# Kernel tuning notes

Measured on AMD Instinct MI355X. Metric: run time of the kernel, lower is better.

The kernel has to match this reference:

```python
import jax, jax.numpy as jnp
import numpy as np

L, D, H, FF = 6, 1024, 16, 4096
HD = D // H
EPS = 1e-5


def _ln(x, g, b):
    m = jnp.mean(x, axis=-1, keepdims=True)
    v = jnp.var(x, axis=-1, keepdims=True)
    return (x - m) * jax.lax.rsqrt(v + EPS) * g + b


def _heads(t, S, B):  # [S,B,D] -> [B*H,S,HD]
    return t.reshape(S, B * H, HD).swapaxes(0, 1)


def _attn(q, k, v, mask):
    # q,k,v: [B*H, Sq/Sk, HD]; q pre-scaled
    scores = jnp.einsum('bqd,bkd->bqk', q, k)
    if mask is not None:
        scores = scores + mask  # broadcast [1,Sq,Sk]
    p = jax.nn.softmax(scores, axis=-1)
    return jnp.einsum('bqk,bkd->bqd', p, v)


def _self_attn(x, w_qkv, b_qkv, w_out, b_out, mask):
    S, B, _ = x.shape
    qkv = x @ w_qkv.T + b_qkv  # [S,B,3D]
    q, k, v = jnp.split(qkv, 3, axis=-1)
    q = q * (HD ** -0.5)
    a = _attn(_heads(q, S, B), _heads(k, S, B), _heads(v, S, B), mask)
    a = a.swapaxes(0, 1).reshape(S, B, D)
    return a @ w_out.T + b_out


def _cross_attn(x, mem, w_q, b_q, w_kv, b_kv, w_out, b_out):
    S, B, _ = x.shape
    Sm = mem.shape[0]
    q = (x @ w_q.T + b_q) * (HD ** -0.5)
    kv = mem @ w_kv.T + b_kv  # [Sm,B,2D]
    k, v = jnp.split(kv, 2, axis=-1)
    a = _attn(_heads(q, S, B), _heads(k, Sm, B), _heads(v, Sm, B), None)
    a = a.swapaxes(0, 1).reshape(S, B, D)
    return a @ w_out.T + b_out


def _ffn(x, w1, b1, w2, b2):
    h = jax.nn.gelu(x @ w1.T + b1, approximate=False)
    return h @ w2.T + b2


def setup_inputs() -> dict:
    key = jax.random.key(0)
    ks = iter(jax.random.split(key, 64))
    def p(*shape, s=0.02):
        return (jax.random.normal(next(ks), shape, dtype=jnp.float32) * s)
    inp = {
        'src': jax.random.normal(next(ks), (512, 8, D), dtype=jnp.float32),
        'tgt': jax.random.normal(next(ks), (512, 8, D), dtype=jnp.float32),
        # encoder params (stacked over L layers)
        'enc_qkv_w': p(L, 3 * D, D), 'enc_qkv_b': p(L, 3 * D),
        'enc_out_w': p(L, D, D), 'enc_out_b': p(L, D),
        'enc_ln1_g': jnp.ones((L, D)), 'enc_ln1_b': jnp.zeros((L, D)),
        'enc_fc1_w': p(L, FF, D), 'enc_fc1_b': p(L, FF),
        'enc_fc2_w': p(L, D, FF), 'enc_fc2_b': p(L, D),
        'enc_ln2_g': jnp.ones((L, D)), 'enc_ln2_b': jnp.zeros((L, D)),
        'enc_norm_g': jnp.ones((D,)), 'enc_norm_b': jnp.zeros((D,)),
        # decoder params
        'dec_qkv_w': p(L, 3 * D, D), 'dec_qkv_b': p(L, 3 * D),
        'dec_sout_w': p(L, D, D), 'dec_sout_b': p(L, D),
        'dec_ln1_g': jnp.ones((L, D)), 'dec_ln1_b': jnp.zeros((L, D)),
        'dec_q_w': p(L, D, D), 'dec_q_b': p(L, D),
        'dec_kv_w': p(L, 2 * D, D), 'dec_kv_b': p(L, 2 * D),
        'dec_cout_w': p(L, D, D), 'dec_cout_b': p(L, D),
        'dec_ln2_g': jnp.ones((L, D)), 'dec_ln2_b': jnp.zeros((L, D)),
        'dec_fc1_w': p(L, FF, D), 'dec_fc1_b': p(L, FF),
        'dec_fc2_w': p(L, D, FF), 'dec_fc2_b': p(L, D),
        'dec_ln3_g': jnp.ones((L, D)), 'dec_ln3_b': jnp.zeros((L, D)),
        'dec_norm_g': jnp.ones((D,)), 'dec_norm_b': jnp.zeros((D,)),
    }
    return inp


def reference(src, tgt,
              enc_qkv_w, enc_qkv_b, enc_out_w, enc_out_b,
              enc_ln1_g, enc_ln1_b, enc_fc1_w, enc_fc1_b,
              enc_fc2_w, enc_fc2_b, enc_ln2_g, enc_ln2_b,
              enc_norm_g, enc_norm_b,
              dec_qkv_w, dec_qkv_b, dec_sout_w, dec_sout_b,
              dec_ln1_g, dec_ln1_b, dec_q_w, dec_q_b,
              dec_kv_w, dec_kv_b, dec_cout_w, dec_cout_b,
              dec_ln2_g, dec_ln2_b, dec_fc1_w, dec_fc1_b,
              dec_fc2_w, dec_fc2_b, dec_ln3_g, dec_ln3_b,
              dec_norm_g, dec_norm_b):
    St = tgt.shape[0]
    # causal additive mask [1,St,St]
    causal = jnp.where(jnp.tril(jnp.ones((St, St), dtype=bool)), 0.0, -jnp.inf)
    causal = causal[None].astype(src.dtype)

    # ---- encoder ----
    x = src
    for i in range(L):
        x = x + _self_attn(_ln(x, enc_ln1_g[i], enc_ln1_b[i]),
                           enc_qkv_w[i], enc_qkv_b[i], enc_out_w[i], enc_out_b[i], None)
        x = x + _ffn(_ln(x, enc_ln2_g[i], enc_ln2_b[i]),
                     enc_fc1_w[i], enc_fc1_b[i], enc_fc2_w[i], enc_fc2_b[i])
    memory = _ln(x, enc_norm_g, enc_norm_b)

    # ---- decoder ----
    y = tgt
    for i in range(L):
        y = y + _self_attn(_ln(y, dec_ln1_g[i], dec_ln1_b[i]),
                           dec_qkv_w[i], dec_qkv_b[i], dec_sout_w[i], dec_sout_b[i], causal)
        y = y + _cross_attn(_ln(y, dec_ln2_g[i], dec_ln2_b[i]), memory,
                            dec_q_w[i], dec_q_b[i], dec_kv_w[i], dec_kv_b[i],
                            dec_cout_w[i], dec_cout_b[i])
        y = y + _ffn(_ln(y, dec_ln3_g[i], dec_ln3_b[i]),
                     dec_fc1_w[i], dec_fc1_b[i], dec_fc2_w[i], dec_fc2_b[i])
    return _ln(y, dec_norm_g, dec_norm_b)
```

## Files before the change

kernel.cpp:

```cpp
#include <hip/hip_runtime.h>

typedef __attribute__((ext_vector_type(4))) float f32x4;
typedef __attribute__((ext_vector_type(8))) short short8;
typedef unsigned int u32;
typedef unsigned short u16;
typedef __attribute__((ext_vector_type(2))) u32 u32x2;
typedef __attribute__((ext_vector_type(4))) u32 u32x4;

#define DEV __device__ __forceinline__
#define SB0  __builtin_amdgcn_sched_barrier(0)
#define HBAR asm volatile("s_barrier" ::: "memory")

DEV u16 f2b(float f){
  u32 u = __builtin_bit_cast(u32, f);
  u32 r = u + 0x7fffu + ((u >> 16) & 1u);
  return (u16)(r >> 16);
}
DEV u32 pk2(float a, float b){ return (u32)f2b(a) | ((u32)f2b(b) << 16); }

DEV void gload16(const void* g, void* l){
  __builtin_amdgcn_global_load_lds((const __attribute__((address_space(1))) void*)g,
                                   (__attribute__((address_space(3))) void*)l, 16, 0, 0);
}
DEV u32 lds_addr(void* p){
  return (u32)(unsigned long long)(__attribute__((address_space(3))) char*)p;
}

__global__ __launch_bounds__(256) void cvt_k(const float* __restrict__ in,
                                             u16* __restrict__ out, int n8)
{
  int i = blockIdx.x*256 + threadIdx.x;
  const int stride = gridDim.x*256;
  for (; i < n8; i += stride){
    const float4 a = ((const float4*)in)[2*i];
    const float4 b = ((const float4*)in)[2*i+1];
    u32x4 r;
    r.x = pk2(a.x,a.y); r.y = pk2(a.z,a.w);
    r.z = pk2(b.x,b.y); r.w = pk2(b.z,b.w);
    ((u32x4*)out)[i] = r;
  }
}

template<int OUT_F32>
__global__ __launch_bounds__(256) void ln_k(const float* __restrict__ x,
    const float* __restrict__ gam, const float* __restrict__ bet,
    void* __restrict__ out)
{
  const int row = blockIdx.x, tid = threadIdx.x;
  const float4 v = ((const float4*)(x + row*1024))[tid];
  float s = (v.x + v.y) + (v.z + v.w);
  float q = (v.x*v.x + v.y*v.y) + (v.z*v.z + v.w*v.w);
  #pragma unroll
  for (int m = 1; m < 64; m <<= 1){ s += __shfl_xor(s, m); q += __shfl_xor(q, m); }
  __shared__ float ps[4], pq[4];
  if ((tid & 63) == 0){ ps[tid>>6] = s; pq[tid>>6] = q; }
  __syncthreads();
  s = (ps[0]+ps[1]) + (ps[2]+ps[3]);
  q = (pq[0]+pq[1]) + (pq[2]+pq[3]);
  const float mean = s * (1.f/1024.f);
  const float var  = q * (1.f/1024.f) - mean*mean;
  const float rstd = rsqrtf(var + 1e-5f);
  const float4 gg = ((const float4*)gam)[tid];
  const float4 bb = ((const float4*)bet)[tid];
  const float o0 = (v.x-mean)*rstd*gg.x + bb.x;
  const float o1 = (v.y-mean)*rstd*gg.y + bb.y;
  const float o2 = (v.z-mean)*rstd*gg.z + bb.z;
  const float o3 = (v.w-mean)*rstd*gg.w + bb.w;
  if (OUT_F32){
    float4 r; r.x=o0; r.y=o1; r.z=o2; r.w=o3;
    ((float4*)out)[row*256 + tid] = r;
  } else {
    u32x2 r; r.x = pk2(o0,o1); r.y = pk2(o2,o3);
    ((u32x2*)out)[row*256 + tid] = r;
  }
}

template<int DO_GELU>
__global__ __launch_bounds__(512,2) void gemm256_k(
    const u16* __restrict__ A, const u16* __restrict__ W,
    const float* __restrict__ bias, u16* __restrict__ Cout,
    int M, int N, int K)
{
  __shared__ char lds[131072];
  const int tid = threadIdx.x;
  const int lane = tid & 63, wid = tid >> 6;
  const int wr = wid >> 2, wc = wid & 3;
  const int g = lane >> 4, c16 = lane & 15;

  const u32 nwg = gridDim.x * gridDim.y;
  u32 flat = blockIdx.x + gridDim.x * blockIdx.y;
  {
    const u32 q = nwg >> 3, r = nwg & 7;
    const u32 xcd = flat & 7, idx = flat >> 3;
    flat = (xcd < r ? xcd*(q+1) : r*(q+1) + (xcd-r)*q) + idx;
  }
  const int m0 = (int)(flat % gridDim.x) * 256;
  const int n0 = (int)(flat / gridDim.x) * 256;

  f32x4 acc[8][4];
  #pragma unroll
  for (int m = 0; m < 8; m++)
    #pragma unroll
    for (int n = 0; n < 4; n++) acc[m][n] = (f32x4){0.f,0.f,0.f,0.f};

  const int srow = tid >> 3, schk = tid & 7;
  const int scg = schk ^ (srow & 7);
  const u16* aS = A + (size_t)(m0 + srow)*K + scg*8;
  const u16* wS = W + (size_t)(n0 + srow)*K + scg*8;

  auto SG = [&](const u16* base, int regionOff, int sb, int half, int i, int kk){
    gload16(base + (size_t)(half*128 + i*64)*K + kk,
            lds + sb*65536 + regionOff + half*16384 + i*8192 + tid*16);
  };
  short8 af[4][2], bf[4][2];
  auto LDA4 = [&](char* bufA, int mbase){
    #pragma unroll
    for (int i = 0; i < 4; i++){
      const int r = (mbase + i)*16 + c16;
      const int rx = r & 7;
      af[i][0] = *(const short8*)(bufA + r*128 + ((g ^ rx) << 4));
      af[i][1] = *(const short8*)(bufA + r*128 + (((4 + g) ^ rx) << 4));
    }
  };
  auto LDB2 = [&](char* bufB, int nbase){
    #pragma unroll
    for (int i = 0; i < 2; i++){
      const int r = (wc & 1)*64 + (nbase + i)*16 + c16;
      const int rx = r & 7;
      bf[nbase+i][0] = *(const short8*)(bufB + r*128 + ((g ^ rx) << 4));
      bf[nbase+i][1] = *(const short8*)(bufB + r*128 + (((4 + g) ^ rx) << 4));
    }
  };

  const int NT = K >> 6;
  SG(wS, 32768, 0, 0, 0, 0); SG(wS, 32768, 0, 0, 1, 0);
  SG(wS, 32768, 0, 1, 0, 0); SG(wS, 32768, 0, 1, 1, 0);
  SG(aS, 0,     0, 0, 0, 0); SG(aS, 0,     0, 0, 1, 0);
  SG(aS, 0,     0, 1, 0, 0); SG(aS, 0,     0, 1, 1, 0);
  asm volatile("s_waitcnt vmcnt(1)" ::: "memory");
  HBAR;

  for (int t = 0; t < NT; ++t){
    const int b = t & 1, sb = b ^ 1;
    const int skk = (t+1) << 6;
    const bool st = (t+1 < NT);
    char* bufA = lds + b*65536 + wr*16384;
    char* bufB = lds + b*65536 + 32768 + (wc >> 1)*16384;

    LDA4(bufA, 0); LDB2(bufB, 0);
    if (st){ SG(wS, 32768, sb, 0, 0, skk); SG(wS, 32768, sb, 0, 1, skk); }
    HBAR;
    asm volatile("s_waitcnt lgkmcnt(0)" ::: "memory"); SB0;
    __builtin_amdgcn_s_setprio(1);
    #pragma unroll
    for (int ks = 0; ks < 2; ks++)
      #pragma unroll
      for (int i = 0; i < 4; i++)
        #pragma unroll
        for (int j = 0; j < 2; j++)
          acc[i][j] = __builtin_amdgcn_mfma_f32_16x16x32_bf16(af[i][ks], bf[j][ks], acc[i][j], 0,0,0);
    __builtin_amdgcn_s_setprio(0);
    LDB2(bufB, 2);
    if (st){ SG(wS, 32768, sb, 1, 0, skk); SG(wS, 32768, sb, 1, 1, skk); }
    HBAR;
    asm volatile("s_waitcnt lgkmcnt(0)" ::: "memory"); SB0;
    __builtin_amdgcn_s_setprio(1);
    #pragma unroll
    for (int ks = 0; ks < 2; ks++)
      #pragma unroll
      for (int i = 0; i < 4; i++)
        #pragma unroll
        for (int j = 2; j < 4; j++)
          acc[i][j] = __builtin_amdgcn_mfma_f32_16x16x32_bf16(af[i][ks], bf[j][ks], acc[i][j], 0,0,0);
    __builtin_amdgcn_s_setprio(0);
    if (st) asm volatile("s_waitcnt vmcnt(4)" ::: "memory");
    else    asm volatile("s_waitcnt vmcnt(0)" ::: "memory");
    HBAR;
    LDA4(bufA, 4);
    if (st){ SG(aS, 0, sb, 0, 0, skk); SG(aS, 0, sb, 0, 1, skk); }
    asm volatile("s_waitcnt lgkmcnt(0)" ::: "memory"); SB0;
    __builtin_amdgcn_s_setprio(1);
    #pragma unroll
    for (int ks = 0; ks < 2; ks++)
      #pragma unroll
      for (int i = 0; i < 4; i++)
        #pragma unroll
        for (int j = 0; j < 2; j++)
          acc[4+i][j] = __builtin_amdgcn_mfma_f32_16x16x32_bf16(af[i][ks], bf[j][ks], acc[4+i][j], 0,0,0);
    __builtin_amdgcn_s_setprio(0);
    if (st){ SG(aS, 0, sb, 1, 0, skk); SG(aS, 0, sb, 1, 1, skk); }
    HBAR;
    __builtin_amdgcn_s_setprio(1);
    #pragma unroll
    for (int ks = 0; ks < 2; ks++)
      #pragma unroll
      for (int i = 0; i < 4; i++)
        #pragma unroll
        for (int j = 2; j < 4; j++)
          acc[4+i][j] = __builtin_amdgcn_mfma_f32_16x16x32_bf16(af[i][ks], bf[j][ks], acc[4+i][j], 0,0,0);
    __builtin_amdgcn_s_setprio(0);
    if (st) asm volatile("s_waitcnt vmcnt(1)" ::: "memory");
    HBAR;
  }

  #pragma unroll
  for (int n = 0; n < 4; n++){
    const int col = n0 + wc*64 + n*16 + c16;
    const float bv = bias[col];
    #pragma unroll
    for (int m = 0; m < 8; m++){
      const int rbase = m0 + wr*128 + m*16 + g*4;
      #pragma unroll
      for (int r = 0; r < 4; r++){
        float v = acc[m][n][r] + bv;
        if (DO_GELU) v = 0.5f*v*(1.f + erff(v*0.70710678118654752f));
        Cout[(size_t)(rbase + r)*N + col] = f2b(v);
      }
    }
  }
}

template<int DO_GELU, int DO_RES, int OUT_F32>
__global__ __launch_bounds__(512,2) void gemm128p_k(
    const u16* __restrict__ A, const u16* __restrict__ W,
    const float* __restrict__ bias, const float* __restrict__ res,
    void* __restrict__ Cout, int M, int N, int K)
{
  __shared__ char lds[65536];
  const int tid = threadIdx.x;
  const int lane = tid & 63, wid = tid >> 6;
  const int wr = wid >> 2, wc = wid & 3;
  const int g = lane >> 4, c16 = lane & 15;

  const u32 nwg = gridDim.x * gridDim.y;
  u32 flat = blockIdx.x + gridDim.x * blockIdx.y;
  {
    const u32 q = nwg >> 3, r = nwg & 7;
    const u32 xcd = flat & 7, idx = flat >> 3;
    flat = (xcd < r ? xcd*(q+1) : r*(q+1) + (xcd-r)*q) + idx;
  }
  const int n0 = (int)(flat % gridDim.x) * 128;
  const int m0 = (int)(flat / gridDim.x) * 128;

  f32x4 acc[4][2];
  #pragma unroll
  for (int m = 0; m < 4; m++)
    #pragma unroll
    for (int n = 0; n < 2; n++) acc[m][n] = (f32x4){0.f,0.f,0.f,0.f};

  const int srow = tid >> 3, schk = tid & 7;
  const int scg = schk ^ (srow & 7);
  const u16* aS = A + (size_t)(m0 + srow)*K + scg*8;
  const u16* wS = W + (size_t)(n0 + srow)*K + scg*8;

  auto SG = [&](const u16* base, int regionOff, int sb, int i, int kk){
    gload16(base + (size_t)(i*64)*K + kk,
            lds + sb*32768 + regionOff + i*8192 + tid*16);
  };
  short8 af[2][2], af2[2][2], bf[2][2];
  auto LDA = [&](short8 (*dst)[2], char* bufA, int mbase){
    #pragma unroll
    for (int i = 0; i < 2; i++){
      const int r = wr*64 + (mbase + i)*16 + c16;
      const int rx = r & 7;
      dst[i][0] = *(const short8*)(bufA + r*128 + ((g ^ rx) << 4));
      dst[i][1] = *(const short8*)(bufA + r*128 + (((4 + g) ^ rx) << 4));
    }
  };
  auto LDB = [&](char* bufB){
    #pragma unroll
    for (int i = 0; i < 2; i++){
      const int r = wc*32 + i*16 + c16;
      const int rx = r & 7;
      bf[i][0] = *(const short8*)(bufB + r*128 + ((g ^ rx) << 4));
      bf[i][1] = *(const short8*)(bufB + r*128 + (((4 + g) ^ rx) << 4));
    }
  };

  const int NT = K >> 6;
  SG(wS, 16384, 0, 0, 0); SG(wS, 16384, 0, 1, 0);
  SG(aS, 0,     0, 0, 0); SG(aS, 0,     0, 1, 0);

  for (int t = 0; t < NT; ++t){
    const int b = t & 1, sb = b ^ 1;
    const int skk = (t+1) << 6;
    const bool st = (t+1 < NT);
    char* bufA = lds + b*32768;
    char* bufB = lds + b*32768 + 16384;

    if (st){ SG(wS, 16384, sb, 0, skk); SG(wS, 16384, sb, 1, skk); }
    if (st) asm volatile("s_waitcnt vmcnt(2)" ::: "memory");
    else    asm volatile("s_waitcnt vmcnt(0)" ::: "memory");
    HBAR;
    LDA(af, bufA, 0); LDB(bufB);
    if (st){ SG(aS, 0, sb, 0, skk); SG(aS, 0, sb, 1, skk); }
    asm volatile("s_waitcnt lgkmcnt(0)" ::: "memory"); SB0;
    __builtin_amdgcn_s_setprio(1);
    #pragma unroll
    for (int ks = 0; ks < 2; ks++)
      #pragma unroll
      for (int i = 0; i < 2; i++)
        #pragma unroll
        for (int j = 0; j < 2; j++)
          acc[i][j] = __builtin_amdgcn_mfma_f32_16x16x32_bf16(af[i][ks], bf[j][ks], acc[i][j], 0,0,0);
    __builtin_amdgcn_s_setprio(0);
    LDA(af2, bufA, 2);
    asm volatile("s_waitcnt lgkmcnt(0)" ::: "memory"); SB0;
    __builtin_amdgcn_s_setprio(1);
    #pragma unroll
    for (int ks = 0; ks < 2; ks++)
      #pragma unroll
      for (int i = 0; i < 2; i++)
        #pragma unroll
        for (int j = 0; j < 2; j++)
          acc[2+i][j] = __builtin_amdgcn_mfma_f32_16x16x32_bf16(af2[i][ks], bf[j][ks], acc[2+i][j], 0,0,0);
    __builtin_amdgcn_s_setprio(0);
    HBAR;
  }

  #pragma unroll
  for (int n = 0; n < 2; n++){
    const int col = n0 + wc*32 + n*16 + c16;
    const float bv = bias[col];
    #pragma unroll
    for (int m = 0; m < 4; m++){
      const int rbase = m0 + wr*64 + m*16 + g*4;
      #pragma unroll
      for (int r = 0; r < 4; r++){
        float v = acc[m][n][r] + bv;
        if (DO_GELU) v = 0.5f*v*(1.f + erff(v*0.70710678118654752f));
        if (DO_RES)  v += res[(size_t)(rbase + r)*N + col];
        if (OUT_F32) ((float*)Cout)[(size_t)(rbase + r)*N + col] = v;
        else         ((u16*)Cout)[(size_t)(rbase + r)*N + col] = f2b(v);
      }
    }
  }
}

template<int CAUSAL>
__global__ __launch_bounds__(256,4) void attn_k(
    const u16* __restrict__ Qb, int qB, int qS,
    const u16* __restrict__ Kb, int kB, int kS,
    const u16* __restrict__ Vb, int vB, int vS,
    u16* __restrict__ Ob, int oB, int oS, float scale)
{
  __shared__ char smem[32768];
  const int tid = threadIdx.x;
  const int lane = tid & 63, w = tid >> 6;
  const int g = lane >> 4, c16 = lane & 15;
  const int qt = blockIdx.x, bh = blockIdx.y;
  const int b = bh >> 4, h = bh & 15;
  const u16* Q  = Qb + b*qB + h*64;
  const u16* Kp = Kb + b*kB + h*64;
  const u16* Vp = Vb + b*vB + h*64;
  u16*       Op = Ob + b*oB + h*64;

  const int qrow = qt*64 + w*16 + c16;
  const short8 bq0 = *(const short8*)(Q + qrow*qS + g*8);
  const short8 bq1 = *(const short8*)(Q + qrow*qS + 32 + g*8);

  f32x4 o[4];
  #pragma unroll
  for (int d = 0; d < 4; d++) o[d] = (f32x4){0.f,0.f,0.f,0.f};
  float mrun = -__builtin_inff(), lrun = 0.f;

  const int srow = tid >> 3, schk = tid & 7;
  const u16* kSrc = Kp + srow*kS + (schk ^ (srow & 7))*8;
  const u16* vSrc = Vp + srow*vS + schk*8;
  const u32 vtr0 = lds_addr(smem) + 16384 + (8*g + (c16 >> 2))*128 + (c16 & 3)*8;

  auto STAGE = [&](int p, int j0){
    char* kb = smem + p*8192 + w*1024;
    char* vb = smem + 16384 + p*8192 + w*1024;
    gload16(kSrc + (size_t)j0*kS, kb);
    gload16(kSrc + (size_t)(j0+32)*kS, kb + 4096);
    gload16(vSrc + (size_t)j0*vS, vb);
    gload16(vSrc + (size_t)(j0+32)*vS, vb + 4096);
  };
  auto COMPUTE = [&](int p, int j0){
    char* Ks = smem + p*8192;
    f32x4 st[4];
    #pragma unroll
    for (int t = 0; t < 4; t++){
      const int row = t*16 + c16;
      const int rx = row & 7;
      const short8 ka0 = *(const short8*)(Ks + row*128 + ((g ^ rx) << 4));
      const short8 ka1 = *(const short8*)(Ks + row*128 + (((4 + g) ^ rx) << 4));
      f32x4 z = (f32x4){0.f,0.f,0.f,0.f};
      z = __builtin_amdgcn_mfma_f32_16x16x32_bf16(ka0, bq0, z, 0,0,0);
      z = __builtin_amdgcn_mfma_f32_16x16x32_bf16(ka1, bq1, z, 0,0,0);
      st[t] = z;
    }
    float mloc = -__builtin_inff();
    #pragma unroll
    for (int t = 0; t < 4; t++)
      #pragma unroll
      for (int r = 0; r < 4; r++){
        float sv = st[t][r]*scale;
        if (CAUSAL){ if (j0 + t*16 + g*4 + r > qrow) sv = -__builtin_inff(); }
        st[t][r] = sv;
        mloc = fmaxf(mloc, sv);
      }
    mloc = fmaxf(mloc, __shfl_xor(mloc, 16));
    mloc = fmaxf(mloc, __shfl_xor(mloc, 32));
    const float mnew = fmaxf(mrun, mloc);
    const float corr = __expf(mrun - mnew);
    float psum = 0.f;
    u32 pk[4][2];
    #pragma unroll
    for (int t = 0; t < 4; t++){
      const float p0 = __expf(st[t][0]-mnew), p1 = __expf(st[t][1]-mnew);
      const float p2 = __expf(st[t][2]-mnew), p3 = __expf(st[t][3]-mnew);
      psum += (p0+p1) + (p2+p3);
      pk[t][0] = pk2(p0,p1); pk[t][1] = pk2(p2,p3);
    }
    psum += __shfl_xor(psum, 16);
    psum += __shfl_xor(psum, 32);
    lrun = lrun*corr + psum;
    mrun = mnew;
    #pragma unroll
    for (int d = 0; d < 4; d++){
      o[d][0]*=corr; o[d][1]*=corr; o[d][2]*=corr; o[d][3]*=corr;
    }
    const int sl0 = c16 | (((g << 1)     & 3) << 4);
    const int sl1 = c16 | ((((g << 1)+1) & 3) << 4);
    const bool hi = g >= 2;
    union { short8 s; u32 u[4]; } pb, pb2;
    {
      const u32 a00 = (u32)__shfl((int)pk[0][0], sl0), a01 = (u32)__shfl((int)pk[0][1], sl0);
      const u32 a02 = (u32)__shfl((int)pk[0][0], sl1), a03 = (u32)__shfl((int)pk[0][1], sl1);
      const u32 a10 = (u32)__shfl((int)pk[1][0], sl0), a11 = (u32)__shfl((int)pk[1][1], sl0);
      const u32 a12 = (u32)__shfl((int)pk[1][0], sl1), a13 = (u32)__shfl((int)pk[1][1], sl1);
      pb.u[0] = hi ? a10 : a00;
      pb.u[1] = hi ? a11 : a01;
      pb.u[2] = hi ? a12 : a02;
      pb.u[3] = hi ? a13 : a03;
    }
    {
      const u32 a00 = (u32)__shfl((int)pk[2][0], sl0), a01 = (u32)__shfl((int)pk[2][1], sl0);
      const u32 a02 = (u32)__shfl((int)pk[2][0], sl1), a03 = (u32)__shfl((int)pk[2][1], sl1);
      const u32 a10 = (u32)__shfl((int)pk[3][0], sl0), a11 = (u32)__shfl((int)pk[3][1], sl0);
      const u32 a12 = (u32)__shfl((int)pk[3][0], sl1), a13 = (u32)__shfl((int)pk[3][1], sl1);
      pb2.u[0] = hi ? a10 : a00;
      pb2.u[1] = hi ? a11 : a01;
      pb2.u[2] = hi ? a12 : a02;
      pb2.u[3] = hi ? a13 : a03;
    }

    const u32 vtr = vtr0 + p*8192;
    u32x2 t00,t01,t10,t11,t20,t21,t30,t31;
    asm volatile("ds_read_b64_tr_b16 %0, %1 offset:0"   : "=v"(t00) : "v"(vtr));
    asm volatile("ds_read_b64_tr_b16 %0, %1 offset:512" : "=v"(t01) : "v"(vtr));
    asm volatile("ds_read_b64_tr_b16 %0, %1 offset:32"  : "=v"(t10) : "v"(vtr));
    asm volatile("ds_read_b64_tr_b16 %0, %1 offset:544" : "=v"(t11) : "v"(vtr));
    asm volatile("ds_read_b64_tr_b16 %0, %1 offset:64"  : "=v"(t20) : "v"(vtr));
    asm volatile("ds_read_b64_tr_b16 %0, %1 offset:576" : "=v"(t21) : "v"(vtr));
    asm volatile("ds_read_b64_tr_b16 %0, %1 offset:96"  : "=v"(t30) : "v"(vtr));
    asm volatile("ds_read_b64_tr_b16 %0, %1 offset:608" : "=v"(t31) : "v"(vtr));
    asm volatile("s_waitcnt lgkmcnt(0)" ::: "memory");
    __builtin_amdgcn_sched_barrier(0);
    {
      union { short8 s; u32x2 d[2]; } v0u, v1u, v2u, v3u;
      v0u.d[0]=t00; v0u.d[1]=t01;
      v1u.d[0]=t10; v1u.d[1]=t11;
      v2u.d[0]=t20; v2u.d[1]=t21;
      v3u.d[0]=t30; v3u.d[1]=t31;
      o[0] = __builtin_amdgcn_mfma_f32_16x16x32_bf16(v0u.s, pb.s, o[0], 0,0,0);
      o[1] = __builtin_amdgcn_mfma_f32_16x16x32_bf16(v1u.s, pb.s, o[1], 0,0,0);
      o[2] = __builtin_amdgcn_mfma_f32_16x16x32_bf16(v2u.s, pb.s, o[2], 0,0,0);
      o[3] = __builtin_amdgcn_mfma_f32_16x16x32_bf16(v3u.s, pb.s, o[3], 0,0,0);
    }
    asm volatile("ds_read_b64_tr_b16 %0, %1 offset:4096" : "=v"(t00) : "v"(vtr));
    asm volatile("ds_read_b64_tr_b16 %0, %1 offset:4608" : "=v"(t01) : "v"(vtr));
    asm volatile("ds_read_b64_tr_b16 %0, %1 offset:4128" : "=v"(t10) : "v"(vtr));
    asm volatile("ds_read_b64_tr_b16 %0, %1 offset:4640" : "=v"(t11) : "v"(vtr));
    asm volatile("ds_read_b64_tr_b16 %0, %1 offset:4160" : "=v"(t20) : "v"(vtr));
    asm volatile("ds_read_b64_tr_b16 %0, %1 offset:4672" : "=v"(t21) : "v"(vtr));
    asm volatile("ds_read_b64_tr_b16 %0, %1 offset:4192" : "=v"(t30) : "v"(vtr));
    asm volatile("ds_read_b64_tr_b16 %0, %1 offset:4704" : "=v"(t31) : "v"(vtr));
    asm volatile("s_waitcnt lgkmcnt(0)" ::: "memory");
    __builtin_amdgcn_sched_barrier(0);
    {
      union { short8 s; u32x2 d[2]; } v0u, v1u, v2u, v3u;
      v0u.d[0]=t00; v0u.d[1]=t01;
      v1u.d[0]=t10; v1u.d[1]=t11;
      v2u.d[0]=t20; v2u.d[1]=t21;
      v3u.d[0]=t30; v3u.d[1]=t31;
      o[0] = __builtin_amdgcn_mfma_f32_16x16x32_bf16(v0u.s, pb2.s, o[0], 0,0,0);
      o[1] = __builtin_amdgcn_mfma_f32_16x16x32_bf16(v1u.s, pb2.s, o[1], 0,0,0);
      o[2] = __builtin_amdgcn_mfma_f32_16x16x32_bf16(v2u.s, pb2.s, o[2], 0,0,0);
      o[3] = __builtin_amdgcn_mfma_f32_16x16x32_bf16(v3u.s, pb2.s, o[3], 0,0,0);
    }
  };

  const int nCh = CAUSAL ? (qt + 1) : 8;
  STAGE(0, 0);
  for (int jc = 0; jc < nCh - 1; ++jc){
    STAGE((jc+1) & 1, (jc+1)*64);
    asm volatile("s_waitcnt vmcnt(4)" ::: "memory");
    HBAR; SB0;
    COMPUTE(jc & 1, jc*64);
    SB0; HBAR;
  }
  asm volatile("s_waitcnt vmcnt(0)" ::: "memory");
  HBAR; SB0;
  COMPUTE((nCh-1) & 1, (nCh-1)*64);
  SB0; HBAR;

  const float inv = 1.f / lrun;
  char* Olds = smem;
  #pragma unroll
  for (int dd = 0; dd < 4; dd++){
    u32x2 val;
    val.x = pk2(o[dd][0]*inv, o[dd][1]*inv);
    val.y = pk2(o[dd][2]*inv, o[dd][3]*inv);
    const int row = w*16 + c16;
    const int off = 32*dd + 8*g;
    const int chunk = off >> 4, rem = off & 15;
    *(u32x2*)(Olds + row*128 + ((chunk ^ (row & 7)) << 4) + rem) = val;
  }
  __syncthreads();
  const int orow = tid >> 2, oc = tid & 3;
  #pragma unroll
  for (int i = 0; i < 2; i++){
    const int ch = oc*2 + i;
    const u32x4 vv = *(const u32x4*)(Olds + orow*128 + ((ch ^ (orow & 7)) << 4));
    *(u32x4*)(Op + (qt*64 + orow)*oS + ch*8) = vv;
  }
}

static inline int cvt_grid(int n8){ int g = (n8 + 255) / 256; return g > 2048 ? 2048 : g; }

extern "C" void kernel_launch(void* const* d_in, const int* in_sizes, int n_in,
                              void* d_out, int out_size, void* d_ws, size_t ws_size,
                              hipStream_t stream)
{
  (void)in_sizes; (void)n_in; (void)out_size; (void)ws_size;
  const float* src      = (const float*)d_in[0];
  const float* tgt      = (const float*)d_in[1];
  const float* e_qkv_w  = (const float*)d_in[2];
  const float* e_qkv_b  = (const float*)d_in[3];
  const float* e_out_w  = (const float*)d_in[4];
  const float* e_out_b  = (const float*)d_in[5];
  const float* e_ln1_g  = (const float*)d_in[6];
  const float* e_ln1_b  = (const float*)d_in[7];
  const float* e_fc1_w  = (const float*)d_in[8];
  const float* e_fc1_b  = (const float*)d_in[9];
  const float* e_fc2_w  = (const float*)d_in[10];
  const float* e_fc2_b  = (const float*)d_in[11];
  const float* e_ln2_g  = (const float*)d_in[12];
  const float* e_ln2_b  = (const float*)d_in[13];
  const float* e_nrm_g  = (const float*)d_in[14];
  const float* e_nrm_b  = (const float*)d_in[15];
  const float* dc_qkv_w = (const float*)d_in[16];
  const float* dc_qkv_b = (const float*)d_in[17];
  const float* dc_sout_w= (const float*)d_in[18];
  const float* dc_sout_b= (const float*)d_in[19];
  const float* dc_ln1_g = (const float*)d_in[20];
  const float* dc_ln1_b = (const float*)d_in[21];
  const float* dc_q_w   = (const float*)d_in[22];
  const float* dc_q_b   = (const float*)d_in[23];
  const float* dc_kv_w  = (const float*)d_in[24];
  const float* dc_kv_b  = (const float*)d_in[25];
  const float* dc_cout_w= (const float*)d_in[26];
  const float* dc_cout_b= (const float*)d_in[27];
  const float* dc_ln2_g = (const float*)d_in[28];
  const float* dc_ln2_b = (const float*)d_in[29];
  const float* dc_fc1_w = (const float*)d_in[30];
  const float* dc_fc1_b = (const float*)d_in[31];
  const float* dc_fc2_w = (const float*)d_in[32];
  const float* dc_fc2_b = (const float*)d_in[33];
  const float* dc_ln3_g = (const float*)d_in[34];
  const float* dc_ln3_b = (const float*)d_in[35];
  const float* dc_nrm_g = (const float*)d_in[36];
  const float* dc_nrm_b = (const float*)d_in[37];

  char* ws = (char*)d_ws;
  u16*  ln_out = (u16*)(ws);
  u16*  attn_o = (u16*)(ws + (8u<<20));
  u16*  membuf = (u16*)(ws + (16u<<20));
  float* xres  = (float*)(ws + (24u<<20));
  u16*  region = (u16*)(ws + (40u<<20));
  u16*  qkv   = region;
  u16*  hbuf  = region;
  u16*  qbuf  = region;
  u16*  kvbuf = region + (4u<<20);

  const dim3 blk(256);
  const dim3 blk512(512);
  const int M = 4096;

  u16* wb = (u16*)(ws + (72u<<20));
  size_t woff = 0;
  auto CV = [&](const float* wsrc, size_t n)->u16* {
    u16* p = wb + woff; woff += n;
    cvt_k<<<cvt_grid((int)(n >> 3)), blk, 0, stream>>>(wsrc, p, (int)(n >> 3));
    return p;
  };
  u16* Weqkv = CV(e_qkv_w,  6ull*3072*1024);
  u16* Weout = CV(e_out_w,  6ull*1024*1024);
  u16* Wefc1 = CV(e_fc1_w,  6ull*4096*1024);
  u16* Wefc2 = CV(e_fc2_w,  6ull*4096*1024);
  u16* Wdqkv = CV(dc_qkv_w, 6ull*3072*1024);
  u16* Wdsout= CV(dc_sout_w,6ull*1024*1024);
  u16* Wdq   = CV(dc_q_w,   6ull*1024*1024);
  u16* Wdkv  = CV(dc_kv_w,  6ull*2048*1024);
  u16* Wdcout= CV(dc_cout_w,6ull*1024*1024);
  u16* Wdfc1 = CV(dc_fc1_w, 6ull*4096*1024);
  u16* Wdfc2 = CV(dc_fc2_w, 6ull*4096*1024);

  for (int i = 0; i < 6; i++){
    const float* xin = i ? xres : src;
    ln_k<0><<<4096, blk, 0, stream>>>(xin, e_ln1_g + i*1024, e_ln1_b + i*1024, ln_out);
    gemm256_k<0><<<dim3(16, 12), blk512, 0, stream>>>(ln_out,
        Weqkv + (size_t)i*3145728, e_qkv_b + i*3072, qkv, M, 3072, 1024);
    attn_k<0><<<dim3(8,128), blk, 0, stream>>>(qkv, 3072, 24576,
        qkv+1024, 3072, 24576, qkv+2048, 3072, 24576, attn_o, 1024, 8192, 0.125f);
    gemm128p_k<0,1,1><<<dim3(8, 32), blk512, 0, stream>>>(attn_o,
        Weout + (size_t)i*1048576, e_out_b + i*1024, xin, xres, M, 1024, 1024);
    ln_k<0><<<4096, blk, 0, stream>>>(xres, e_ln2_g + i*1024, e_ln2_b + i*1024, ln_out);
    gemm256_k<1><<<dim3(16, 16), blk512, 0, stream>>>(ln_out,
        Wefc1 + (size_t)i*4194304, e_fc1_b + i*4096, hbuf, M, 4096, 1024);
    gemm128p_k<0,1,1><<<dim3(8, 32), blk512, 0, stream>>>(hbuf,
        Wefc2 + (size_t)i*4194304, e_fc2_b + i*1024, xres, xres, M, 1024, 4096);
  }
  ln_k<0><<<4096, blk, 0, stream>>>(xres, e_nrm_g, e_nrm_b, membuf);

  for (int i = 0; i < 6; i++){
    const float* yin = i ? xres : tgt;
    ln_k<0><<<4096, blk, 0, stream>>>(yin, dc_ln1_g + i*1024, dc_ln1_b + i*1024, ln_out);
    gemm256_k<0><<<dim3(16, 12), blk512, 0, stream>>>(ln_out,
        Wdqkv + (size_t)i*3145728, dc_qkv_b + i*3072, qkv, M, 3072, 1024);
    attn_k<1><<<dim3(8,128), blk, 0, stream>>>(qkv, 3072, 24576,
        qkv+1024, 3072, 24576, qkv+2048, 3072, 24576, attn_o, 1024, 8192, 0.125f);
    gemm128p_k<0,1,1><<<dim3(8, 32), blk512, 0, stream>>>(attn_o,
        Wdsout + (size_t)i*1048576, dc_sout_b + i*1024, yin, xres, M, 1024, 1024);
    ln_k<0><<<4096, blk, 0, stream>>>(xres, dc_ln2_g + i*1024, dc_ln2_b + i*1024, ln_out);
    gemm128p_k<0,0,0><<<dim3(8, 32), blk512, 0, stream>>>(ln_out,
        Wdq + (size_t)i*1048576, dc_q_b + i*1024, nullptr, qbuf, M, 1024, 1024);
    gemm128p_k<0,0,0><<<dim3(16, 32), blk512, 0, stream>>>(membuf,
        Wdkv + (size_t)i*2097152, dc_kv_b + i*2048, nullptr, kvbuf, M, 2048, 1024);
    attn_k<0><<<dim3(8,128), blk, 0, stream>>>(qbuf, 1024, 8192,
        kvbuf, 2048, 16384, kvbuf+1024, 2048, 16384, attn_o, 1024, 8192, 0.125f);
    gemm128p_k<0,1,1><<<dim3(8, 32), blk512, 0, stream>>>(attn_o,
        Wdcout + (size_t)i*1048576, dc_cout_b + i*1024, xres, xres, M, 1024, 1024);
    ln_k<0><<<4096, blk, 0, stream>>>(xres, dc_ln3_g + i*1024, dc_ln3_b + i*1024, ln_out);
    gemm256_k<1><<<dim3(16, 16), blk512, 0, stream>>>(ln_out,
        Wdfc1 + (size_t)i*4194304, dc_fc1_b + i*4096, hbuf, M, 4096, 1024);
    gemm128p_k<0,1,1><<<dim3(8, 32), blk512, 0, stream>>>(hbuf,
        Wdfc2 + (size_t)i*4194304, dc_fc2_b + i*1024, xres, xres, M, 1024, 4096);
  }
  ln_k<1><<<4096, blk, 0, stream>>>(xres, dc_nrm_g, dc_nrm_b, d_out);
}
```

Measured before the change: 3.193 ms.

## Split-K the FFN down-projection GEMM with a separate reduction kernel

Replaces the fc2 GEMM (K=4096, N=1024) with a split-K variant that splits K into four 1024-wide slices across grid z. Each slice writes fp32 partials, and a new reduction kernel sums them with bias and residual. This quadruples the number of workgroups for a GEMM that otherwise launches only 256 tiles, improving CU occupancy on a large-CU GPU. The cost is 64MB of extra fp32 partial writes and reads per layer, plus one extra launch.

```diff
diff --git a/kernel.cpp b/kernel.cpp
--- a/kernel.cpp
+++ b/kernel.cpp
@@ -75,6 +75,26 @@
   }
 }
 
+__global__ __launch_bounds__(256) void reduce4_k(const float* __restrict__ p,
+    const float* __restrict__ res, const float* __restrict__ bias,
+    float* __restrict__ out)
+{
+  const int row = blockIdx.x, tid = threadIdx.x;
+  const size_t MN = 4096ull*1024ull;
+  const float4 b  = ((const float4*)bias)[tid];
+  const float4 a0 = ((const float4*)(p + 0*MN + (size_t)row*1024))[tid];
+  const float4 a1 = ((const float4*)(p + 1*MN + (size_t)row*1024))[tid];
+  const float4 a2 = ((const float4*)(p + 2*MN + (size_t)row*1024))[tid];
+  const float4 a3 = ((const float4*)(p + 3*MN + (size_t)row*1024))[tid];
+  const float4 r  = ((const float4*)(res + (size_t)row*1024))[tid];
+  float4 o;
+  o.x = (a0.x+a1.x)+(a2.x+a3.x) + r.x + b.x;
+  o.y = (a0.y+a1.y)+(a2.y+a3.y) + r.y + b.y;
+  o.z = (a0.z+a1.z)+(a2.z+a3.z) + r.z + b.z;
+  o.w = (a0.w+a1.w)+(a2.w+a3.w) + r.w + b.w;
+  ((float4*)(out + (size_t)row*1024))[tid] = o;
+}
+
 template<int DO_GELU>
 __global__ __launch_bounds__(512,2) void gemm256_k(
     const u16* __restrict__ A, const u16* __restrict__ W,
@@ -333,6 +353,117 @@
         if (OUT_F32) ((float*)Cout)[(size_t)(rbase + r)*N + col] = v;
         else         ((u16*)Cout)[(size_t)(rbase + r)*N + col] = f2b(v);
       }
+    }
+  }
+}
+
+__global__ __launch_bounds__(512,2) void gemmsk_k(
+    const u16* __restrict__ A, const u16* __restrict__ W,
+    float* __restrict__ part, int M, int N, int Kfull)
+{
+  __shared__ char lds[65536];
+  const int tid = threadIdx.x;
+  const int lane = tid & 63, wid = tid >> 6;
+  const int wr = wid >> 2, wc = wid & 3;
+  const int g = lane >> 4, c16 = lane & 15;
+  const int k0 = (int)blockIdx.z << 10;
+
+  const u32 nwg = gridDim.x * gridDim.y;
+  u32 flat = blockIdx.x + gridDim.x * blockIdx.y;
+  {
+    const u32 q = nwg >> 3, r = nwg & 7;
+    const u32 xcd = flat & 7, idx = flat >> 3;
+    flat = (xcd < r ? xcd*(q+1) : r*(q+1) + (xcd-r)*q) + idx;
+  }
+  const int n0 = (int)(flat % gridDim.x) * 128;
+  const int m0 = (int)(flat / gridDim.x) * 128;
+
+  f32x4 acc[4][2];
+  #pragma unroll
+  for (int m = 0; m < 4; m++)
+    #pragma unroll
+    for (int n = 0; n < 2; n++) acc[m][n] = (f32x4){0.f,0.f,0.f,0.f};
+
+  const int srow = tid >> 3, schk = tid & 7;
+  const int scg = schk ^ (srow & 7);
+  const u16* aS = A + (size_t)(m0 + srow)*Kfull + k0 + scg*8;
+  const u16* wS = W + (size_t)(n0 + srow)*Kfull + k0 + scg*8;
+
+  auto SG = [&](const u16* base, int regionOff, int sb, int i, int kk){
+    gload16(base + (size_t)(i*64)*Kfull + kk,
+            lds + sb*32768 + regionOff + i*8192 + tid*16);
+  };
+  short8 af[2][2], af2[2][2], bf[2][2];
+  auto LDA = [&](short8 (*dst)[2], char* bufA, int mbase){
+    #pragma unroll
+    for (int i = 0; i < 2; i++){
+      const int r = wr*64 + (mbase + i)*16 + c16;
+      const int rx = r & 7;
+      dst[i][0] = *(const short8*)(bufA + r*128 + ((g ^ rx) << 4));
+      dst[i][1] = *(const short8*)(bufA + r*128 + (((4 + g) ^ rx) << 4));
+    }
+  };
+  auto LDB = [&](char* bufB){
+    #pragma unroll
+    for (int i = 0; i < 2; i++){
+      const int r = wc*32 + i*16 + c16;
+      const int rx = r & 7;
+      bf[i][0] = *(const short8*)(bufB + r*128 + ((g ^ rx) << 4));
+      bf[i][1] = *(const short8*)(bufB + r*128 + (((4 + g) ^ rx) << 4));
+    }
+  };
+
+  const int NT = 16;
+  SG(wS, 16384, 0, 0, 0); SG(wS, 16384, 0, 1, 0);
+  SG(aS, 0,     0, 0, 0); SG(aS, 0,     0, 1, 0);
+
+  for (int t = 0; t < NT; ++t){
+    const int b = t & 1, sb = b ^ 1;
+    const int skk = (t+1) << 6;
+    const bool st = (t+1 < NT);
+    char* bufA = lds + b*32768;
+    char* bufB = lds + b*32768 + 16384;
+
+    if (st){ SG(wS, 16384, sb, 0, skk); SG(wS, 16384, sb, 1, skk); }
+    if (st) asm volatile("s_waitcnt vmcnt(2)" ::: "memory");
+    else    asm volatile("s_waitcnt vmcnt(0)" ::: "memory");
+    HBAR;
+    LDA(af, bufA, 0); LDB(bufB);
+    if (st){ SG(aS, 0, sb, 0, skk); SG(aS, 0, sb, 1, skk); }
+    asm volatile("s_waitcnt lgkmcnt(0)" ::: "memory"); SB0;
+    __builtin_amdgcn_s_setprio(1);
+    #pragma unroll
+    for (int ks = 0; ks < 2; ks++)
+      #pragma unroll
+      for (int i = 0; i < 2; i++)
+        #pragma unroll
+        for (int j = 0; j < 2; j++)
+          acc[i][j] = __builtin_amdgcn_mfma_f32_16x16x32_bf16(af[i][ks], bf[j][ks], acc[i][j], 0,0,0);
+    __builtin_amdgcn_s_setprio(0);
+    LDA(af2, bufA, 2);
+    asm volatile("s_waitcnt lgkmcnt(0)" ::: "memory"); SB0;
+    __builtin_amdgcn_s_setprio(1);
+    #pragma unroll
+    for (int ks = 0; ks < 2; ks++)
+      #pragma unroll
+      for (int i = 0; i < 2; i++)
+        #pragma unroll
+        for (int j = 0; j < 2; j++)
+          acc[2+i][j] = __builtin_amdgcn_mfma_f32_16x16x32_bf16(af2[i][ks], bf[j][ks], acc[2+i][j], 0,0,0);
+    __builtin_amdgcn_s_setprio(0);
+    HBAR;
+  }
+
+  float* out = part + (size_t)blockIdx.z * ((size_t)M * N);
+  #pragma unroll
+  for (int n = 0; n < 2; n++){
+    const int col = n0 + wc*32 + n*16 + c16;
+    #pragma unroll
+    for (int m = 0; m < 4; m++){
+      const int rbase = m0 + wr*64 + m*16 + g*4;
+      #pragma unroll
+      for (int r = 0; r < 4; r++)
+        out[(size_t)(rbase + r)*N + col] = acc[m][n][r];
     }
   }
 }
@@ -585,6 +716,7 @@
   u16*  hbuf  = region;
   u16*  qbuf  = region;
   u16*  kvbuf = region + (4u<<20);
+  float* fparts = (float*)(ws + (432ull<<20));
 
   const dim3 blk(256);
   const dim3 blk512(512);
@@ -621,8 +753,9 @@
     ln_k<0><<<4096, blk, 0, stream>>>(xres, e_ln2_g + i*1024, e_ln2_b + i*1024, ln_out);
     gemm256_k<1><<<dim3(16, 16), blk512, 0, stream>>>(ln_out,
         Wefc1 + (size_t)i*4194304, e_fc1_b + i*4096, hbuf, M, 4096, 1024);
-    gemm128p_k<0,1,1><<<dim3(8, 32), blk512, 0, stream>>>(hbuf,
-        Wefc2 + (size_t)i*4194304, e_fc2_b + i*1024, xres, xres, M, 1024, 4096);
+    gemmsk_k<<<dim3(8, 32, 4), blk512, 0, stream>>>(hbuf,
+        Wefc2 + (size_t)i*4194304, fparts, M, 1024, 4096);
+    reduce4_k<<<4096, blk, 0, stream>>>(fparts, xres, e_fc2_b + i*1024, xres);
   }
   ln_k<0><<<4096, blk, 0, stream>>>(xres, e_nrm_g, e_nrm_b, membuf);
 
@@ -647,8 +780,9 @@
     ln_k<0><<<4096, blk, 0, stream>>>(xres, dc_ln3_g + i*1024, dc_ln3_b + i*1024, ln_out);
     gemm256_k<1><<<dim3(16, 16), blk512, 0, stream>>>(ln_out,
         Wdfc1 + (size_t)i*4194304, dc_fc1_b + i*4096, hbuf, M, 4096, 1024);
-    gemm128p_k<0,1,1><<<dim3(8, 32), blk512, 0, stream>>>(hbuf,
-        Wdfc2 + (size_t)i*4194304, dc_fc2_b + i*1024, xres, xres, M, 1024, 4096);
+    gemmsk_k<<<dim3(8, 32, 4), blk512, 0, stream>>>(hbuf,
+        Wdfc2 + (size_t)i*4194304, fparts, M, 1024, 4096);
+    reduce4_k<<<4096, blk, 0, stream>>>(fparts, xres, dc_fc2_b + i*1024, xres);
   }
   ln_k<1><<<4096, blk, 0, stream>>>(xres, dc_nrm_g, dc_nrm_b, d_out);
 }
```

Result: slower. 3.362 ms (+5.3%).

## Batch cross-attention KV projections for all decoder layers into one GEMM

Applied to the files above, without the earlier changes.

Merges the eleven per-tensor weight conversion launches into one segmented conversion kernel. Hoists the six per-layer cross-attention K/V projections of the encoder memory out of the decoder loop into a single wide GEMM (N=12288) whose output is kept in a large workspace buffer. Attention then reads K/V with a 12288-element row stride. This trades extra workspace memory and a strided K/V access pattern for fewer launches and better GEMM utilisation. The attention staging pointers are widened to size_t because of the larger offsets.

```diff
diff --git a/kernel.cpp b/kernel.cpp
--- a/kernel.cpp
+++ b/kernel.cpp
@@ -26,18 +26,24 @@
   return (u32)(unsigned long long)(__attribute__((address_space(3))) char*)p;
 }
 
-__global__ __launch_bounds__(256) void cvt_k(const float* __restrict__ in,
-                                             u16* __restrict__ out, int n8)
+struct CvtSegs { const float* src[11]; u32 cum[12]; };
+
+__global__ __launch_bounds__(256) void cvtall_k(CvtSegs segs,
+    u16* __restrict__ dst, int total8)
 {
   int i = blockIdx.x*256 + threadIdx.x;
   const int stride = gridDim.x*256;
-  for (; i < n8; i += stride){
-    const float4 a = ((const float4*)in)[2*i];
-    const float4 b = ((const float4*)in)[2*i+1];
+  for (; i < total8; i += stride){
+    int seg = 0;
+    #pragma unroll
+    for (int s = 1; s < 11; s++) if ((u32)i >= segs.cum[s]) seg = s;
+    const float* sp = segs.src[seg] + (size_t)((u32)i - segs.cum[seg])*8;
+    const float4 a = ((const float4*)sp)[0];
+    const float4 b = ((const float4*)sp)[1];
     u32x4 r;
     r.x = pk2(a.x,a.y); r.y = pk2(a.z,a.w);
     r.z = pk2(b.x,b.y); r.w = pk2(b.z,b.w);
-    ((u32x4*)out)[i] = r;
+    ((u32x4*)dst)[i] = r;
   }
 }
 
@@ -365,8 +371,8 @@
   float mrun = -__builtin_inff(), lrun = 0.f;
 
   const int srow = tid >> 3, schk = tid & 7;
-  const u16* kSrc = Kp + srow*kS + (schk ^ (srow & 7))*8;
-  const u16* vSrc = Vp + srow*vS + schk*8;
+  const u16* kSrc = Kp + (size_t)srow*kS + (schk ^ (srow & 7))*8;
+  const u16* vSrc = Vp + (size_t)srow*vS + schk*8;
   const u32 vtr0 = lds_addr(smem) + 16384 + (8*g + (c16 >> 2))*128 + (c16 & 3)*8;
 
   auto STAGE = [&](int p, int j0){
@@ -528,8 +534,6 @@
     *(u32x4*)(Op + (qt*64 + orow)*oS + ch*8) = vv;
   }
 }
-
-static inline int cvt_grid(int n8){ int g = (n8 + 255) / 256; return g > 2048 ? 2048 : g; }
 
 extern "C" void kernel_launch(void* const* d_in, const int* in_sizes, int n_in,
                               void* d_out, int out_size, void* d_ws, size_t ws_size,
@@ -584,30 +588,38 @@
   u16*  qkv   = region;
   u16*  hbuf  = region;
   u16*  qbuf  = region;
-  u16*  kvbuf = region + (4u<<20);
+  u16*  wb    = (u16*)(ws + (72u<<20));
+  u16*  kvall = (u16*)(ws + (424ull<<20));
 
   const dim3 blk(256);
   const dim3 blk512(512);
   const int M = 4096;
 
-  u16* wb = (u16*)(ws + (72u<<20));
+  CvtSegs segs;
   size_t woff = 0;
-  auto CV = [&](const float* wsrc, size_t n)->u16* {
-    u16* p = wb + woff; woff += n;
-    cvt_k<<<cvt_grid((int)(n >> 3)), blk, 0, stream>>>(wsrc, p, (int)(n >> 3));
+  u32 cum8 = 0;
+  int nseg = 0;
+  auto REG = [&](const float* srcp, size_t n)->u16* {
+    u16* p = wb + woff;
+    segs.src[nseg] = srcp;
+    segs.cum[nseg] = cum8;
+    nseg++;
+    woff += n; cum8 += (u32)(n >> 3);
     return p;
   };
-  u16* Weqkv = CV(e_qkv_w,  6ull*3072*1024);
-  u16* Weout = CV(e_out_w,  6ull*1024*1024);
-  u16* Wefc1 = CV(e_fc1_w,  6ull*4096*1024);
-  u16* Wefc2 = CV(e_fc2_w,  6ull*4096*1024);
-  u16* Wdqkv = CV(dc_qkv_w, 6ull*3072*1024);
-  u16* Wdsout= CV(dc_sout_w,6ull*1024*1024);
-  u16* Wdq   = CV(dc_q_w,   6ull*1024*1024);
-  u16* Wdkv  = CV(dc_kv_w,  6ull*2048*1024);
-  u16* Wdcout= CV(dc_cout_w,6ull*1024*1024);
-  u16* Wdfc1 = CV(dc_fc1_w, 6ull*4096*1024);
-  u16* Wdfc2 = CV(dc_fc2_w, 6ull*4096*1024);
+  u16* Weqkv = REG(e_qkv_w,  6ull*3072*1024);
+  u16* Weout = REG(e_out_w,  6ull*1024*1024);
+  u16* Wefc1 = REG(e_fc1_w,  6ull*4096*1024);
+  u16* Wefc2 = REG(e_fc2_w,  6ull*4096*1024);
+  u16* Wdqkv = REG(dc_qkv_w, 6ull*3072*1024);
+  u16* Wdsout= REG(dc_sout_w,6ull*1024*1024);
+  u16* Wdq   = REG(dc_q_w,   6ull*1024*1024);
+  u16* Wdkv  = REG(dc_kv_w,  6ull*2048*1024);
+  u16* Wdcout= REG(dc_cout_w,6ull*1024*1024);
+  u16* Wdfc1 = REG(dc_fc1_w, 6ull*4096*1024);
+  u16* Wdfc2 = REG(dc_fc2_w, 6ull*4096*1024);
+  segs.cum[11] = cum8;
+  cvtall_k<<<2048, blk, 0, stream>>>(segs, wb, (int)cum8);
 
   for (int i = 0; i < 6; i++){
     const float* xin = i ? xres : src;
@@ -626,6 +638,9 @@
   }
   ln_k<0><<<4096, blk, 0, stream>>>(xres, e_nrm_g, e_nrm_b, membuf);
 
+  gemm256_k<0><<<dim3(16, 48), blk512, 0, stream>>>(membuf,
+      Wdkv, dc_kv_b, kvall, M, 12288, 1024);
+
   for (int i = 0; i < 6; i++){
     const float* yin = i ? xres : tgt;
     ln_k<0><<<4096, blk, 0, stream>>>(yin, dc_ln1_g + i*1024, dc_ln1_b + i*1024, ln_out);
@@ -638,10 +653,9 @@
     ln_k<0><<<4096, blk, 0, stream>>>(xres, dc_ln2_g + i*1024, dc_ln2_b + i*1024, ln_out);
     gemm128p_k<0,0,0><<<dim3(8, 32), blk512, 0, stream>>>(ln_out,
         Wdq + (size_t)i*1048576, dc_q_b + i*1024, nullptr, qbuf, M, 1024, 1024);
-    gemm128p_k<0,0,0><<<dim3(16, 32), blk512, 0, stream>>>(membuf,
-        Wdkv + (size_t)i*2097152, dc_kv_b + i*2048, nullptr, kvbuf, M, 2048, 1024);
     attn_k<0><<<dim3(8,128), blk, 0, stream>>>(qbuf, 1024, 8192,
-        kvbuf, 2048, 16384, kvbuf+1024, 2048, 16384, attn_o, 1024, 8192, 0.125f);
+        kvall + i*2048, 12288, 98304, kvall + i*2048 + 1024, 12288, 98304,
+        attn_o, 1024, 8192, 0.125f);
     gemm128p_k<0,1,1><<<dim3(8, 32), blk512, 0, stream>>>(attn_o,
         Wdcout + (size_t)i*1048576, dc_cout_b + i*1024, xres, xres, M, 1024, 1024);
     ln_k<0><<<4096, blk, 0, stream>>>(xres, dc_ln3_g + i*1024, dc_ln3_b + i*1024, ln_out);
```

Result: no change. 3.162 ms (-1.0%).
